# Performance work log

Hardware: AMD Instinct MI355X
Metric: run time of the kernel (lower is better)

The kernel has to match this reference:

```python
import jax, jax.numpy as jnp
import numpy as np

NU = 100000  # user nodes
NI = 100000  # item nodes
D_IN = 128
D_OUT = 128
E = 800000   # edges per canonical etype


def setup_inputs() -> dict:
    key = jax.random.key(0)
    ks = jax.random.split(key, 14)
    s = 1.0 / np.sqrt(D_IN)
    return {
        "feat_user": jax.random.normal(ks[0], (NU, D_IN), jnp.float32),
        "feat_item": jax.random.normal(ks[1], (NI, D_IN), jnp.float32),
        "W_follows": jax.random.normal(ks[2], (D_OUT, D_IN), jnp.float32) * s,
        "b_follows": jax.random.normal(ks[3], (D_OUT,), jnp.float32) * s,
        "W_rates": jax.random.normal(ks[4], (D_OUT, D_IN), jnp.float32) * s,
        "b_rates": jax.random.normal(ks[5], (D_OUT,), jnp.float32) * s,
        "W_ratedby": jax.random.normal(ks[6], (D_OUT, D_IN), jnp.float32) * s,
        "b_ratedby": jax.random.normal(ks[7], (D_OUT,), jnp.float32) * s,
        "src_follows": jax.random.randint(ks[8], (E,), 0, NU),
        "dst_follows": jax.random.randint(ks[9], (E,), 0, NU),
        "src_rates": jax.random.randint(ks[10], (E,), 0, NU),
        "dst_rates": jax.random.randint(ks[11], (E,), 0, NI),
        "src_ratedby": jax.random.randint(ks[12], (E,), 0, NI),
        "dst_ratedby": jax.random.randint(ks[13], (E,), 0, NU),
    }


def _mean_agg(Wh, src, dst, n_dst):
    # gather transformed src features per edge, segment-mean over dst
    msg = Wh[src]  # [E, D_OUT]
    s = jax.ops.segment_sum(msg, dst, num_segments=n_dst)
    cnt = jax.ops.segment_sum(jnp.ones((dst.shape[0],), Wh.dtype), dst,
                              num_segments=n_dst)
    return s / jnp.maximum(cnt, 1.0)[:, None]  # zero-degree -> 0, like DGL


def reference(feat_user, feat_item, W_follows, b_follows, W_rates, b_rates,
              W_ratedby, b_ratedby, src_follows, dst_follows, src_rates,
              dst_rates, src_ratedby, dst_ratedby):
    # per-etype linear transform of source node features (Wh)
    Wh_f = feat_user @ W_follows.T + b_follows    # user -> user
    Wh_r = feat_user @ W_rates.T + b_rates        # user -> item
    Wh_rb = feat_item @ W_ratedby.T + b_ratedby   # item -> user
    # copy_u/mean per etype, then 'sum' combine across etypes per dst ntype
    h_user = (_mean_agg(Wh_f, src_follows, dst_follows, NU)
              + _mean_agg(Wh_rb, src_ratedby, dst_ratedby, NU))
    h_item = _mean_agg(Wh_r, src_rates, dst_rates, NI)
    return (h_user, h_item)
```

## Files before the change

### kernel.cpp

```cpp
#include <hip/hip_runtime.h>

#define NU 100000
#define NI 100000
#define DF 128
#define CAP 32
#define BCAP 768
#define NBKT 1600
#define CHUNK 4096

typedef __attribute__((ext_vector_type(8))) short bf16x8;
typedef __attribute__((ext_vector_type(4))) float f32x4;

__device__ __forceinline__ unsigned short f2bf(float f) {
    unsigned u = __float_as_uint(f);
    return (unsigned short)((u + 0x7fffu + ((u >> 16) & 1u)) >> 16);
}
__device__ __forceinline__ float bflo(unsigned v) { return __uint_as_float(v << 16); }
__device__ __forceinline__ float bfhi(unsigned v) { return __uint_as_float(v & 0xffff0000u); }

__global__ void wcvt_kernel(const float* __restrict__ W0,
                            const float* __restrict__ W1,
                            const float* __restrict__ W2,
                            unsigned short* __restrict__ out)
{
    const int i = blockIdx.x * 256 + threadIdx.x;
    const float* src = (i < 16384) ? W0 : ((i < 32768) ? W1 : W2);
    out[i] = f2bf(src[i & 16383]);
}

__device__ __forceinline__ void load_afrag(const float* __restrict__ A,
                                           int row0, int q, int n,
                                           bf16x8 afrag[2][4])
{
#pragma unroll
    for (int t = 0; t < 2; ++t) {
        const float* ap = A + (size_t)(row0 + t * 16 + n) * DF + q * 8;
#pragma unroll
        for (int s = 0; s < 4; ++s) {
            const float4 f0 = *(const float4*)(ap + s * 32);
            const float4 f1 = *(const float4*)(ap + s * 32 + 4);
            bf16x8 fr;
            fr[0] = (short)f2bf(f0.x); fr[1] = (short)f2bf(f0.y);
            fr[2] = (short)f2bf(f0.z); fr[3] = (short)f2bf(f0.w);
            fr[4] = (short)f2bf(f1.x); fr[5] = (short)f2bf(f1.y);
            fr[6] = (short)f2bf(f1.z); fr[7] = (short)f2bf(f1.w);
            afrag[t][s] = fr;
        }
    }
}

__device__ __forceinline__ void mat_pass(const bf16x8 afrag[2][4],
                                         const unsigned short* __restrict__ Wbp,
                                         const float* __restrict__ bias,
                                         unsigned short* __restrict__ Wh,
                                         int row0, int q, int n)
{
#pragma unroll 1
    for (int c = 0; c < 8; ++c) {
        const unsigned short* wp = Wbp + (size_t)(c * 16 + n) * DF + q * 8;
        bf16x8 bfrag[4];
#pragma unroll
        for (int s = 0; s < 4; ++s)
            bfrag[s] = *(const bf16x8*)(wp + s * 32);

        f32x4 acc0 = {0.f, 0.f, 0.f, 0.f};
        f32x4 acc1 = {0.f, 0.f, 0.f, 0.f};
#pragma unroll
        for (int s = 0; s < 4; ++s) {
            acc0 = __builtin_amdgcn_mfma_f32_16x16x32_bf16(afrag[0][s], bfrag[s], acc0, 0, 0, 0);
            acc1 = __builtin_amdgcn_mfma_f32_16x16x32_bf16(afrag[1][s], bfrag[s], acc1, 0, 0, 0);
        }

        const float bv = bias[c * 16 + n];
#pragma unroll
        for (int i = 0; i < 4; ++i) {
            Wh[(size_t)(row0 + q * 4 + i) * DF + c * 16 + n]      = f2bf(acc0[i] + bv);
            Wh[(size_t)(row0 + 16 + q * 4 + i) * DF + c * 16 + n] = f2bf(acc1[i] + bv);
        }
    }
}

__global__ __launch_bounds__(256)
void gemm3_kernel(const float* __restrict__ Au, const float* __restrict__ Ai,
                  const unsigned short* __restrict__ Wb,
                  const float* __restrict__ b_f, const float* __restrict__ b_r,
                  const float* __restrict__ b_rb,
                  unsigned short* __restrict__ Wh_f,
                  unsigned short* __restrict__ Wh_r,
                  unsigned short* __restrict__ Wh_rb, int M)
{
    const int lane = threadIdx.x & 63;
    const int wv   = threadIdx.x >> 6;
    const int q    = lane >> 4;
    const int n    = lane & 15;
    const int row0 = blockIdx.x * 128 + wv * 32;
    if (row0 >= M) return;

    bf16x8 afrag[2][4];
    load_afrag(Au, row0, q, n, afrag);
    mat_pass(afrag, Wb,             b_f, Wh_f, row0, q, n);
    mat_pass(afrag, Wb + 2 * 16384, b_r, Wh_r, row0, q, n);
    load_afrag(Ai, row0, q, n, afrag);
    mat_pass(afrag, Wb + 16384,     b_rb, Wh_rb, row0, q, n);
}

__global__ __launch_bounds__(256)
void bin3_kernel(const int* __restrict__ src0, const int* __restrict__ dst0, int n0, int nb0,
                 const int* __restrict__ src1, const int* __restrict__ dst1, int n1, int nb1,
                 const int* __restrict__ src2, const int* __restrict__ dst2, int n2,
                 int* __restrict__ bcnt, unsigned* __restrict__ pairs)
{
    __shared__ int hist[NBKT];
    const int tid = threadIdx.x;
    int b = blockIdx.x, e;
    const int* src; const int* dst; int n;
    if (b < nb0)            { e = 0; src = src0; dst = dst0; n = n0; }
    else if (b < nb0 + nb1) { b -= nb0; e = 1; src = src1; dst = dst1; n = n1; }
    else                    { b -= nb0 + nb1; e = 2; src = src2; dst = dst2; n = n2; }
    const int base = b * CHUNK;
    int* bc = bcnt + e * NBKT * 16;
    unsigned* pr = pairs + (size_t)e * NBKT * BCAP;

    for (int j = tid; j < NBKT; j += 256) hist[j] = 0;
    __syncthreads();

    unsigned pk[16];
    int meta[16];
#pragma unroll
    for (int k = 0; k < 16; ++k) {
        const int i = base + k * 256 + tid;
        if (i < n) {
            const unsigned d = (unsigned)dst[i];
            const unsigned s = (unsigned)src[i];
            pk[k] = (s << 6) | (d & 63u);
            const int p = atomicAdd(&hist[d >> 6], 1);
            meta[k] = (int)((d >> 6) << 16) | p;
        } else meta[k] = -1;
    }
    __syncthreads();
    for (int j = tid; j < NBKT; j += 256) {
        const int c = hist[j];
        hist[j] = (c > 0) ? atomicAdd(&bc[j * 16], c) : 0;
    }
    __syncthreads();
#pragma unroll
    for (int k = 0; k < 16; ++k) {
        if (meta[k] >= 0) {
            const int bkt = meta[k] >> 16;
            const int p = hist[bkt] + (meta[k] & 0xffff);
            if (p < BCAP) pr[(size_t)bkt * BCAP + p] = pk[k];
        }
    }
}

__device__ __forceinline__ void accum8(const uint4 u, float acc[8]) {
    acc[0] += bflo(u.x); acc[1] += bfhi(u.x);
    acc[2] += bflo(u.y); acc[3] += bfhi(u.y);
    acc[4] += bflo(u.z); acc[5] += bfhi(u.z);
    acc[6] += bflo(u.w); acc[7] += bfhi(u.w);
}

__device__ __forceinline__ void gather_q(const unsigned short* __restrict__ Wh,
                                         int s, int d, int dmax,
                                         int selbase, int qh, int c16,
                                         float acc[8])
{
    for (int j = 0; j < dmax; j += 4) {
        const int e0 = j + qh;
        const int e1 = j + 2 + qh;
        const int id0 = __shfl(s, selbase + e0, 64);
        const int id1 = __shfl(s, selbase + e1, 64);
        if (e0 < d) accum8(*((const uint4*)(Wh + (size_t)id0 * DF) + c16), acc);
        if (e1 < d) accum8(*((const uint4*)(Wh + (size_t)id1 * DF) + c16), acc);
    }
}

__global__ __launch_bounds__(256, 8)
void bagg_kernel(const unsigned short* __restrict__ Wh_f,
                 const unsigned short* __restrict__ Wh_rb,
                 const unsigned short* __restrict__ Wh_r,
                 const int* __restrict__ bcnt, const unsigned* __restrict__ pairs,
                 float* __restrict__ out_user, float* __restrict__ out_item,
                 int nbu)
{
    __shared__ int cntA[64], cntB[64];
    __shared__ unsigned slotA[64 * CAP], slotB[64 * CAP];
    const int tid = threadIdx.x;
    const bool user = (blockIdx.x < nbu);
    const int bkt = user ? blockIdx.x : blockIdx.x - nbu;

    if (tid < 64) { cntA[tid] = 0; cntB[tid] = 0; }
    __syncthreads();

    const int wv = tid >> 6, lane = tid & 63;
    const int c16 = lane & 15;
    const int qh = (lane >> 4) & 1;
    const int h = lane >> 5;
    const int selbase = lane & 32;

    if (user) {
        const int nf  = min(bcnt[0 * NBKT * 16 + bkt * 16], BCAP);
        const int nrb = min(bcnt[1 * NBKT * 16 + bkt * 16], BCAP);
        const unsigned* prf  = pairs + (size_t)bkt * BCAP;
        const unsigned* prrb = pairs + (size_t)NBKT * BCAP + (size_t)bkt * BCAP;
        for (int i = tid; i < nf; i += 256) {
            const unsigned v = prf[i];
            const int dl = v & 63;
            const int p = atomicAdd(&cntA[dl], 1);
            if (p < CAP) slotA[dl * CAP + p] = v >> 6;
        }
        for (int i = tid; i < nrb; i += 256) {
            const unsigned v = prrb[i];
            const int dl = v & 63;
            const int p = atomicAdd(&cntB[dl], 1);
            if (p < CAP) slotB[dl * CAP + p] = v >> 6;
        }
        __syncthreads();

        for (int t = 0; t < 8; ++t) {
            const int dl = wv * 16 + t * 2 + h;
            const int node = bkt * 64 + dl;
            const int degf  = cntA[dl];
            const int degrb = cntB[dl];
            const int sf  = (int)slotA[dl * CAP + (lane & 31)];
            const int srb = (int)slotB[dl * CAP + (lane & 31)];
            const int df  = min(degf, CAP);
            const int drb = min(degrb, CAP);
            const int dfm  = max(df,  __shfl_xor(df, 32, 64));
            const int drbm = max(drb, __shfl_xor(drb, 32, 64));

            float acc[8];
#pragma unroll
            for (int k = 0; k < 8; ++k) acc[k] = 0.f;
            gather_q(Wh_f, sf, df, dfm, selbase, qh, c16, acc);
            const float invf = degf > 0 ? 1.f / (float)degf : 0.f;
            float res[8];
#pragma unroll
            for (int k = 0; k < 8; ++k) { res[k] = acc[k] * invf; acc[k] = 0.f; }

            gather_q(Wh_rb, srb, drb, drbm, selbase, qh, c16, acc);
            const float invrb = degrb > 0 ? 1.f / (float)degrb : 0.f;
#pragma unroll
            for (int k = 0; k < 8; ++k) {
                res[k] += acc[k] * invrb;
                res[k] += __shfl_xor(res[k], 16, 64);
            }
            if (!(lane & 16) && node < NU) {
                float* op = out_user + (size_t)node * DF + c16 * 8;
                float4 o0 = {res[0], res[1], res[2], res[3]};
                float4 o1 = {res[4], res[5], res[6], res[7]};
                *(float4*)op = o0;
                *((float4*)op + 1) = o1;
            }
        }
    } else {
        const int nr = min(bcnt[2 * NBKT * 16 + bkt * 16], BCAP);
        const unsigned* prr = pairs + 2 * (size_t)NBKT * BCAP + (size_t)bkt * BCAP;
        for (int i = tid; i < nr; i += 256) {
            const unsigned v = prr[i];
            const int dl = v & 63;
            const int p = atomicAdd(&cntA[dl], 1);
            if (p < CAP) slotA[dl * CAP + p] = v >> 6;
        }
        __syncthreads();

        for (int t = 0; t < 8; ++t) {
            const int dl = wv * 16 + t * 2 + h;
            const int node = bkt * 64 + dl;
            const int degr = cntA[dl];
            const int sr = (int)slotA[dl * CAP + (lane & 31)];
            const int dr = min(degr, CAP);
            const int drm = max(dr, __shfl_xor(dr, 32, 64));

            float acc[8];
#pragma unroll
            for (int k = 0; k < 8; ++k) acc[k] = 0.f;
            gather_q(Wh_r, sr, dr, drm, selbase, qh, c16, acc);
            const float invr = degr > 0 ? 1.f / (float)degr : 0.f;
            float res[8];
#pragma unroll
            for (int k = 0; k < 8; ++k) {
                res[k] = acc[k] * invr;
                res[k] += __shfl_xor(res[k], 16, 64);
            }
            if (!(lane & 16) && node < NI) {
                float* op = out_item + (size_t)node * DF + c16 * 8;
                float4 o0 = {res[0], res[1], res[2], res[3]};
                float4 o1 = {res[4], res[5], res[6], res[7]};
                *(float4*)op = o0;
                *((float4*)op + 1) = o1;
            }
        }
    }
}

extern "C" void kernel_launch(void* const* d_in, const int* in_sizes, int n_in,
                              void* d_out, int out_size, void* d_ws,
                              size_t ws_size, hipStream_t stream)
{
    const float* feat_user = (const float*)d_in[0];
    const float* feat_item = (const float*)d_in[1];
    const float* W_f  = (const float*)d_in[2];
    const float* b_f  = (const float*)d_in[3];
    const float* W_r  = (const float*)d_in[4];
    const float* b_r  = (const float*)d_in[5];
    const float* W_rb = (const float*)d_in[6];
    const float* b_rb = (const float*)d_in[7];
    const int* src_f  = (const int*)d_in[8];
    const int* dst_f  = (const int*)d_in[9];
    const int* src_r  = (const int*)d_in[10];
    const int* dst_r  = (const int*)d_in[11];
    const int* src_rb = (const int*)d_in[12];
    const int* dst_rb = (const int*)d_in[13];
    const int Ef  = in_sizes[8];
    const int Er  = in_sizes[10];
    const int Erb = in_sizes[12];

    float* out_user = (float*)d_out;
    float* out_item = (float*)d_out + (size_t)NU * DF;

    char* p = (char*)d_ws;
    unsigned short* Wh_f  = (unsigned short*)p;  p += (size_t)NU * DF * 2;
    unsigned short* Wh_rb = (unsigned short*)p;  p += (size_t)NI * DF * 2;
    unsigned short* Wh_r  = (unsigned short*)p;  p += (size_t)NU * DF * 2;
    unsigned* pairs = (unsigned*)p;  p += 3 * (size_t)NBKT * BCAP * 4;
    int* bcnt = (int*)p;             p += 3 * (size_t)NBKT * 16 * 4;
    unsigned short* Wb = (unsigned short*)p;

    wcvt_kernel<<<192, 256, 0, stream>>>(W_f, W_rb, W_r, Wb);
    hipMemsetAsync(bcnt, 0, 3 * (size_t)NBKT * 16 * 4, stream);

    gemm3_kernel<<<(NU + 127) / 128, 256, 0, stream>>>(
        feat_user, feat_item, Wb, b_f, b_r, b_rb, Wh_f, Wh_r, Wh_rb, NU);

    const int nb_f  = (Ef  + CHUNK - 1) / CHUNK;
    const int nb_rb = (Erb + CHUNK - 1) / CHUNK;
    const int nb_r  = (Er  + CHUNK - 1) / CHUNK;
    bin3_kernel<<<nb_f + nb_rb + nb_r, 256, 0, stream>>>(
        src_f,  dst_f,  Ef,  nb_f,
        src_rb, dst_rb, Erb, nb_rb,
        src_r,  dst_r,  Er,  bcnt, pairs);

    const int nbu = (NU + 63) / 64;
    const int nbi = (NI + 63) / 64;
    bagg_kernel<<<nbu + nbi, 256, 0, stream>>>(
        Wh_f, Wh_rb, Wh_r, bcnt, pairs, out_user, out_item, nbu);
}
```

Before: 416.9 us.

## Stage GEMM output via swizzled LDS, unroll gather loads, fuse memset, interleave agg blocks

The GEMM now writes each 128x128 bf16 tile into a swizzled shared-memory buffer and flushes it with coalesced 16-byte row stores, replacing the scattered 2-byte global stores. The aggregation gather reads neighbour IDs straight from LDS and issues four independent row loads per iteration instead of shuffling IDs and doing two loads, which raises memory-level parallelism. The bucket-count memset is folded into the weight-conversion kernel, dropping one launch. User and item aggregation blocks are interleaved so both kinds are in flight together. The costs are an extra 32KB of LDS and more barriers in the GEMM, which may lower occupancy there.

```diff
diff --git a/kernel.cpp b/kernel.cpp
--- a/kernel.cpp
+++ b/kernel.cpp
@@ -21,20 +21,25 @@
 __global__ void wcvt_kernel(const float* __restrict__ W0,
                             const float* __restrict__ W1,
                             const float* __restrict__ W2,
-                            unsigned short* __restrict__ out)
+                            unsigned short* __restrict__ out,
+                            int* __restrict__ bcnt)
 {
     const int i = blockIdx.x * 256 + threadIdx.x;
-    const float* src = (i < 16384) ? W0 : ((i < 32768) ? W1 : W2);
-    out[i] = f2bf(src[i & 16383]);
+    if (i < 3 * 16384) {
+        const float* src = (i < 16384) ? W0 : ((i < 32768) ? W1 : W2);
+        out[i] = f2bf(src[i & 16383]);
+    }
+    if (i < 3 * NBKT * 16) bcnt[i] = 0;
 }
 
 __device__ __forceinline__ void load_afrag(const float* __restrict__ A,
-                                           int row0, int q, int n,
+                                           int row0, int q, int n, int M,
                                            bf16x8 afrag[2][4])
 {
 #pragma unroll
     for (int t = 0; t < 2; ++t) {
-        const float* ap = A + (size_t)(row0 + t * 16 + n) * DF + q * 8;
+        const int rr = min(row0 + t * 16 + n, M - 1);
+        const float* ap = A + (size_t)rr * DF + q * 8;
 #pragma unroll
         for (int s = 0; s < 4; ++s) {
             const float4 f0 = *(const float4*)(ap + s * 32);
@@ -52,8 +57,8 @@
 __device__ __forceinline__ void mat_pass(const bf16x8 afrag[2][4],
                                          const unsigned short* __restrict__ Wbp,
                                          const float* __restrict__ bias,
-                                         unsigned short* __restrict__ Wh,
-                                         int row0, int q, int n)
+                                         unsigned short* __restrict__ ot,
+                                         int wv, int q, int n)
 {
 #pragma unroll 1
     for (int c = 0; c < 8; ++c) {
@@ -72,12 +77,32 @@
         }
 
         const float bv = bias[c * 16 + n];
+        const int col2 = (c * 16 + n) * 2;
 #pragma unroll
         for (int i = 0; i < 4; ++i) {
-            Wh[(size_t)(row0 + q * 4 + i) * DF + c * 16 + n]      = f2bf(acc0[i] + bv);
-            Wh[(size_t)(row0 + 16 + q * 4 + i) * DF + c * 16 + n] = f2bf(acc1[i] + bv);
-        }
-    }
+            const int r0 = wv * 32 + q * 4 + i;
+            const int swz = (r0 & 7) << 4;
+            *(unsigned short*)((char*)ot + ((r0 * 256 + col2) ^ swz))       = f2bf(acc0[i] + bv);
+            *(unsigned short*)((char*)ot + (((r0 + 16) * 256 + col2) ^ swz)) = f2bf(acc1[i] + bv);
+        }
+    }
+}
+
+__device__ __forceinline__ void flush_tile(const unsigned short* __restrict__ ot,
+                                           unsigned short* __restrict__ Wh,
+                                           int rowbase, int M, int tid)
+{
+    __syncthreads();
+#pragma unroll
+    for (int it = 0; it < 8; ++it) {
+        const int chunk = it * 256 + tid;
+        const int row = chunk >> 4;
+        const int lbyte = chunk * 16;
+        const uint4 v = *(const uint4*)((const char*)ot + (lbyte ^ ((row & 7) << 4)));
+        if (rowbase + row < M)
+            *(uint4*)((char*)Wh + (size_t)(rowbase + row) * 256 + (lbyte & 255)) = v;
+    }
+    __syncthreads();
 }
 
 __global__ __launch_bounds__(256)
@@ -89,19 +114,23 @@
                   unsigned short* __restrict__ Wh_r,
                   unsigned short* __restrict__ Wh_rb, int M)
 {
-    const int lane = threadIdx.x & 63;
-    const int wv   = threadIdx.x >> 6;
+    __shared__ unsigned short ot[128 * 128];
+    const int tid  = threadIdx.x;
+    const int lane = tid & 63;
+    const int wv   = tid >> 6;
     const int q    = lane >> 4;
     const int n    = lane & 15;
     const int row0 = blockIdx.x * 128 + wv * 32;
-    if (row0 >= M) return;
 
     bf16x8 afrag[2][4];
-    load_afrag(Au, row0, q, n, afrag);
-    mat_pass(afrag, Wb,             b_f, Wh_f, row0, q, n);
-    mat_pass(afrag, Wb + 2 * 16384, b_r, Wh_r, row0, q, n);
-    load_afrag(Ai, row0, q, n, afrag);
-    mat_pass(afrag, Wb + 16384,     b_rb, Wh_rb, row0, q, n);
+    load_afrag(Au, row0, q, n, M, afrag);
+    mat_pass(afrag, Wb,             b_f, ot, wv, q, n);
+    flush_tile(ot, Wh_f, blockIdx.x * 128, M, tid);
+    mat_pass(afrag, Wb + 2 * 16384, b_r, ot, wv, q, n);
+    flush_tile(ot, Wh_r, blockIdx.x * 128, M, tid);
+    load_afrag(Ai, row0, q, n, M, afrag);
+    mat_pass(afrag, Wb + 16384,     b_rb, ot, wv, q, n);
+    flush_tile(ot, Wh_rb, blockIdx.x * 128, M, tid);
 }
 
 __global__ __launch_bounds__(256)
@@ -161,17 +190,18 @@
 }
 
 __device__ __forceinline__ void gather_q(const unsigned short* __restrict__ Wh,
-                                         int s, int d, int dmax,
-                                         int selbase, int qh, int c16,
-                                         float acc[8])
-{
-    for (int j = 0; j < dmax; j += 4) {
-        const int e0 = j + qh;
-        const int e1 = j + 2 + qh;
-        const int id0 = __shfl(s, selbase + e0, 64);
-        const int id1 = __shfl(s, selbase + e1, 64);
-        if (e0 < d) accum8(*((const uint4*)(Wh + (size_t)id0 * DF) + c16), acc);
-        if (e1 < d) accum8(*((const uint4*)(Wh + (size_t)id1 * DF) + c16), acc);
+                                         const unsigned* __restrict__ sl,
+                                         int d, int qh, int c16, float acc[8])
+{
+    for (int j = 0; j < d; j += 8) {
+        const int e0 = j + qh, e1 = j + 2 + qh, e2 = j + 4 + qh, e3 = j + 6 + qh;
+        uint4 u0 = {0,0,0,0}, u1 = {0,0,0,0}, u2 = {0,0,0,0}, u3 = {0,0,0,0};
+        if (e0 < d) u0 = *((const uint4*)(Wh + (size_t)sl[e0] * DF) + c16);
+        if (e1 < d) u1 = *((const uint4*)(Wh + (size_t)sl[e1] * DF) + c16);
+        if (e2 < d) u2 = *((const uint4*)(Wh + (size_t)sl[e2] * DF) + c16);
+        if (e3 < d) u3 = *((const uint4*)(Wh + (size_t)sl[e3] * DF) + c16);
+        accum8(u0, acc); accum8(u1, acc);
+        accum8(u2, acc); accum8(u3, acc);
     }
 }
 
@@ -180,14 +210,13 @@
                  const unsigned short* __restrict__ Wh_rb,
                  const unsigned short* __restrict__ Wh_r,
                  const int* __restrict__ bcnt, const unsigned* __restrict__ pairs,
-                 float* __restrict__ out_user, float* __restrict__ out_item,
-                 int nbu)
+                 float* __restrict__ out_user, float* __restrict__ out_item)
 {
     __shared__ int cntA[64], cntB[64];
     __shared__ unsigned slotA[64 * CAP], slotB[64 * CAP];
     const int tid = threadIdx.x;
-    const bool user = (blockIdx.x < nbu);
-    const int bkt = user ? blockIdx.x : blockIdx.x - nbu;
+    const bool user = (blockIdx.x & 1) == 0;
+    const int bkt = blockIdx.x >> 1;
 
     if (tid < 64) { cntA[tid] = 0; cntB[tid] = 0; }
     __syncthreads();
@@ -196,7 +225,6 @@
     const int c16 = lane & 15;
     const int qh = (lane >> 4) & 1;
     const int h = lane >> 5;
-    const int selbase = lane & 32;
 
     if (user) {
         const int nf  = min(bcnt[0 * NBKT * 16 + bkt * 16], BCAP);
@@ -222,23 +250,19 @@
             const int node = bkt * 64 + dl;
             const int degf  = cntA[dl];
             const int degrb = cntB[dl];
-            const int sf  = (int)slotA[dl * CAP + (lane & 31)];
-            const int srb = (int)slotB[dl * CAP + (lane & 31)];
             const int df  = min(degf, CAP);
             const int drb = min(degrb, CAP);
-            const int dfm  = max(df,  __shfl_xor(df, 32, 64));
-            const int drbm = max(drb, __shfl_xor(drb, 32, 64));
 
             float acc[8];
 #pragma unroll
             for (int k = 0; k < 8; ++k) acc[k] = 0.f;
-            gather_q(Wh_f, sf, df, dfm, selbase, qh, c16, acc);
+            gather_q(Wh_f, &slotA[dl * CAP], df, qh, c16, acc);
             const float invf = degf > 0 ? 1.f / (float)degf : 0.f;
             float res[8];
 #pragma unroll
             for (int k = 0; k < 8; ++k) { res[k] = acc[k] * invf; acc[k] = 0.f; }
 
-            gather_q(Wh_rb, srb, drb, drbm, selbase, qh, c16, acc);
+            gather_q(Wh_rb, &slotB[dl * CAP], drb, qh, c16, acc);
             const float invrb = degrb > 0 ? 1.f / (float)degrb : 0.f;
 #pragma unroll
             for (int k = 0; k < 8; ++k) {
@@ -268,14 +292,12 @@
             const int dl = wv * 16 + t * 2 + h;
             const int node = bkt * 64 + dl;
             const int degr = cntA[dl];
-            const int sr = (int)slotA[dl * CAP + (lane & 31)];
             const int dr = min(degr, CAP);
-            const int drm = max(dr, __shfl_xor(dr, 32, 64));
 
             float acc[8];
 #pragma unroll
             for (int k = 0; k < 8; ++k) acc[k] = 0.f;
-            gather_q(Wh_r, sr, dr, drm, selbase, qh, c16, acc);
+            gather_q(Wh_r, &slotA[dl * CAP], dr, qh, c16, acc);
             const float invr = degr > 0 ? 1.f / (float)degr : 0.f;
             float res[8];
 #pragma unroll
@@ -327,8 +349,7 @@
     int* bcnt = (int*)p;             p += 3 * (size_t)NBKT * 16 * 4;
     unsigned short* Wb = (unsigned short*)p;
 
-    wcvt_kernel<<<192, 256, 0, stream>>>(W_f, W_rb, W_r, Wb);
-    hipMemsetAsync(bcnt, 0, 3 * (size_t)NBKT * 16 * 4, stream);
+    wcvt_kernel<<<300, 256, 0, stream>>>(W_f, W_rb, W_r, Wb, bcnt);
 
     gemm3_kernel<<<(NU + 127) / 128, 256, 0, stream>>>(
         feat_user, feat_item, Wb, b_f, b_r, b_rb, Wh_f, Wh_r, Wh_rb, NU);
@@ -342,7 +363,6 @@
         src_r,  dst_r,  Er,  bcnt, pairs);
 
     const int nbu = (NU + 63) / 64;
-    const int nbi = (NI + 63) / 64;
-    bagg_kernel<<<nbu + nbi, 256, 0, stream>>>(
-        Wh_f, Wh_rb, Wh_r, bcnt, pairs, out_user, out_item, nbu);
-}
+    bagg_kernel<<<2 * nbu, 256, 0, stream>>>(
+        Wh_f, Wh_rb, Wh_r, bcnt, pairs, out_user, out_item);
+}
```

New measurement: 409.5 us. About the same (-1.8%).
